# Kernel optimization log

Hardware: AMD Instinct MI355X
Metric: run time of the kernel (lower is better)

## Reference

```python
import jax, jax.numpy as jnp
import numpy as np
from jax import lax

V, VE, DE, DX, HID, T, S = 100000, 1000, 256, 64, 512, 64, 2048
H = HID // 2


def setup_inputs() -> dict:
    key = jax.random.key(0)
    ks = jax.random.split(key, 18)
    def n(k, shape, scale=0.1):
        return jax.random.normal(k, shape, jnp.float32) * scale
    return {
        "sentence": jax.random.randint(ks[0], (S,), 0, V),
        "extra": jax.random.randint(ks[1], (S,), 0, VE),
        "b": 0,
        "e": S,
        "emb": n(ks[2], (V, DE)),
        "extra_emb": n(ks[3], (VE, DX)),
        "w_ih_f": n(ks[4], (4 * H, DE + DX)),
        "w_hh_f": n(ks[5], (4 * H, H)),
        "b_ih_f": n(ks[6], (4 * H,)),
        "b_hh_f": n(ks[7], (4 * H,)),
        "w_ih_b": n(ks[8], (4 * H, DE + DX)),
        "w_hh_b": n(ks[9], (4 * H, H)),
        "b_ih_b": n(ks[10], (4 * H,)),
        "b_hh_b": n(ks[11], (4 * H,)),
        "fc_w": n(ks[12], (T, HID)),
        "fc_b": n(ks[13], (T,)),
        "crf_start": n(ks[14], (T,)),
        "crf_end": n(ks[15], (T,)),
        "crf_trans": n(ks[16], (T, T)),
    }


def _lstm_dir(x, w_ih, w_hh, b_ih, b_hh):
    """Single-direction LSTM over x [S, D] with batch 1. PyTorch gate order i,f,g,o."""
    Hh = w_hh.shape[1]
    gx = x @ w_ih.T + (b_ih + b_hh)  # [S, 4H], input projection hoisted out of the scan

    def step(carry, g_in):
        h, c = carry
        g = g_in + h @ w_hh.T  # [4H]
        i, f, gg, o = jnp.split(g, 4)
        i = jax.nn.sigmoid(i)
        f = jax.nn.sigmoid(f)
        gg = jnp.tanh(gg)
        o = jax.nn.sigmoid(o)
        c = f * c + i * gg
        h = o * jnp.tanh(c)
        return (h, c), h

    init = (jnp.zeros((Hh,), x.dtype), jnp.zeros((Hh,), x.dtype))
    _, hs = lax.scan(step, init, gx)
    return hs  # [S, H]


def _lstm_feats(sentence, extra, emb, extra_emb,
                w_ih_f, w_hh_f, b_ih_f, b_hh_f,
                w_ih_b, w_hh_b, b_ih_b, b_hh_b, fc_w, fc_b):
    x = jnp.concatenate([emb[sentence], extra_emb[extra]], axis=1)  # [S, DE+DX]
    hf = _lstm_dir(x, w_ih_f, w_hh_f, b_ih_f, b_hh_f)              # [S, H]
    hb = _lstm_dir(x[::-1], w_ih_b, w_hh_b, b_ih_b, b_hh_b)[::-1]  # [S, H]
    lstm_out = jnp.concatenate([hf, hb], axis=1)                   # [S, 2H]
    return lstm_out @ fc_w.T + fc_b                                # [S, T]


def _viterbi_decode(feats, start, end, trans):
    """torchcrf-style Viterbi on feats [L, T]; returns best tag path [L] (int32)."""
    score0 = start + feats[0]  # [T]

    def step(score, emit_t):
        m = score[:, None] + trans + emit_t[None, :]  # [T_prev, T_next]
        return jnp.max(m, axis=0), jnp.argmax(m, axis=0).astype(jnp.int32)

    final_score, bps = lax.scan(step, score0, feats[1:])  # bps: [L-1, T]
    final_score = final_score + end
    last_tag = jnp.argmax(final_score).astype(jnp.int32)

    def back(tag, bp_t):
        prev = bp_t[tag]
        return prev, prev

    _, prev_tags = lax.scan(back, last_tag, bps[::-1])
    return jnp.concatenate([prev_tags[::-1], last_tag[None]])  # [L]


def reference(sentence, extra, b, e, emb, extra_emb,
              w_ih_f, w_hh_f, b_ih_f, b_hh_f,
              w_ih_b, w_hh_b, b_ih_b, b_hh_b,
              fc_w, fc_b, crf_start, crf_end, crf_trans):
    feats = _lstm_feats(sentence, extra, emb, extra_emb,
                        w_ih_f, w_hh_f, b_ih_f, b_hh_f,
                        w_ih_b, w_hh_b, b_ih_b, b_hh_b, fc_w, fc_b)
    feats = feats[b:e]  # static Python-int phrase bounds
    return _viterbi_decode(feats, crf_start, crf_end, crf_trans)
```

## Files before the change

kernel.cpp:

```cpp
#include <hip/hip_runtime.h>
#include <stdint.h>

#define SEQ   2048
#define DE    256
#define DXX   64
#define DIN   320
#define HH    256
#define G4    1024
#define NT    64

static constexpr size_t OFF_GX = 0;
static constexpr size_t OFF_H  = OFF_GX + (size_t)2 * SEQ * G4;
static constexpr size_t HSTR   = (size_t)SEQ * HH;
static constexpr size_t OFF_SL = OFF_H + 2 * HSTR;
static constexpr size_t OFF_FE = OFF_SL + 2048;
static constexpr size_t OFF_BP = OFF_FE + (size_t)SEQ * NT;
static constexpr size_t WS_NEEDED_BYTES = OFF_BP * 4 + (size_t)SEQ * NT;

__global__ __launch_bounds__(256) void k_init(unsigned long long* __restrict__ slot) {
  const int tid = threadIdx.x;
  #pragma unroll
  for (int b = 0; b < 4; ++b) slot[b * 256 + tid] = 0ull;
}

__global__ __launch_bounds__(512) void k_gx(
    const int* __restrict__ sent, const int* __restrict__ extra,
    const float* __restrict__ emb, const float* __restrict__ xemb,
    const float* __restrict__ wf, const float* __restrict__ wb,
    const float* __restrict__ bif, const float* __restrict__ bhf,
    const float* __restrict__ bib, const float* __restrict__ bhb,
    float* __restrict__ GX) {
  __shared__ __align__(16) float xs[32][36];
  __shared__ __align__(16) float wl[32][260];
  const int tid = threadIdx.x;
  const int s0 = blockIdx.x * 32, r0 = blockIdx.y * 256, dir = blockIdx.z;
  const float* W = dir ? wb : wf;
  const int tids = tid & 7;
  const int tidr = tid >> 3;
  float acc[4][4];
  #pragma unroll
  for (int a = 0; a < 4; ++a)
    #pragma unroll
    for (int b = 0; b < 4; ++b) acc[a][b] = 0.f;

  for (int kc = 0; kc < 10; ++kc) {
    const int k0 = kc * 32;
    __syncthreads();
    for (int e = tid; e < 1024; e += 512) {
      int kk = e & 31, sl = e >> 5;
      int s = s0 + sl;
      int src = dir ? (SEQ - 1 - s) : s;
      int k = k0 + kk;
      float v;
      if (k < DE) v = emb[(size_t)sent[src] * DE + k];
      else        v = xemb[(size_t)extra[src] * DXX + (k - DE)];
      xs[kk][sl] = v;
    }
    for (int e = tid; e < 8192; e += 512) {
      int kk = e & 31, rl = e >> 5;
      wl[kk][rl] = W[(size_t)(r0 + rl) * DIN + k0 + kk];
    }
    __syncthreads();
    #pragma unroll
    for (int kk = 0; kk < 32; ++kk) {
      float4 xv = *(const float4*)&xs[kk][4 * tids];
      float4 wv = *(const float4*)&wl[kk][4 * tidr];
      acc[0][0] += xv.x * wv.x; acc[0][1] += xv.x * wv.y; acc[0][2] += xv.x * wv.z; acc[0][3] += xv.x * wv.w;
      acc[1][0] += xv.y * wv.x; acc[1][1] += xv.y * wv.y; acc[1][2] += xv.y * wv.z; acc[1][3] += xv.y * wv.w;
      acc[2][0] += xv.z * wv.x; acc[2][1] += xv.z * wv.y; acc[2][2] += xv.z * wv.z; acc[2][3] += xv.z * wv.w;
      acc[3][0] += xv.w * wv.x; acc[3][1] += xv.w * wv.y; acc[3][2] += xv.w * wv.z; acc[3][3] += xv.w * wv.w;
    }
  }
  const float* BI = dir ? bib : bif;
  const float* BH = dir ? bhb : bhf;
  float4 b1 = *(const float4*)&BI[r0 + 4 * tidr];
  float4 b2 = *(const float4*)&BH[r0 + 4 * tidr];
  float bx = b1.x + b2.x, by = b1.y + b2.y, bz = b1.z + b2.z, bw = b1.w + b2.w;
  #pragma unroll
  for (int ss = 0; ss < 4; ++ss) {
    int s = s0 + 4 * tids + ss;
    float4 o;
    o.x = acc[ss][0] + bx; o.y = acc[ss][1] + by; o.z = acc[ss][2] + bz; o.w = acc[ss][3] + bw;
    *(float4*)&GX[((size_t)dir * SEQ + s) * G4 + r0 + 4 * tidr] = o;
  }
}

__global__ __launch_bounds__(256, 1) void k_lstm16(
    const float* __restrict__ whf, const float* __restrict__ whb,
    const float* __restrict__ GX, float* __restrict__ H,
    unsigned long long* __restrict__ slot) {
  const int dir = blockIdx.x >> 4;
  const int p   = blockIdx.x & 15;
  const int tid = threadIdx.x;
  const int rr  = tid >> 2;
  const int q   = tid & 3;
  const int gq  = rr >> 4;
  const int joq = rr & 15;
  const int rowQ = (gq << 8) | (p << 4) | joq;
  const int rowC = ((tid >> 4) << 8) | (p << 4) | (tid & 15);

  const float4* w4g =
      (const float4*)((dir ? whb : whf) + (size_t)rowQ * HH) + q * 16;
  float4 w[16];
  #pragma unroll
  for (int i = 0; i < 16; ++i) w[i] = w4g[i];
  #pragma unroll
  for (int i = 0; i < 16; ++i)
    asm volatile("" : "+v"(w[i].x), "+v"(w[i].y), "+v"(w[i].z), "+v"(w[i].w));

  const float* gxc = GX + (size_t)dir * SEQ * G4 + rowC;
  float* Hd = H + (size_t)dir * HSTR;
  unsigned long long* sl = slot + dir * 512;

  __shared__ __align__(16) float hl[4][68];
  __shared__ float psum[256];
  float c = 0.f;
  int budget = 1 << 18;
  const bool ownpoll = ((tid >> 4) == p);

  if (ownpoll) hl[tid >> 6][tid & 63] = 0.f;

  for (int t = 0; t < SEQ; ++t) {
    float gxv = 0.f;
    if (tid < 64) gxv = gxc[(size_t)t * G4];
    if (!ownpoll) {
      unsigned long long* sp = &sl[(t & 1) * 256 + tid];
      const unsigned tw = (unsigned)t;
      unsigned long long v;
      unsigned long long v0 = __hip_atomic_load(sp, __ATOMIC_RELAXED, __HIP_MEMORY_SCOPE_AGENT);
      unsigned long long v1 = __hip_atomic_load(sp, __ATOMIC_RELAXED, __HIP_MEMORY_SCOPE_AGENT);
      unsigned long long v2 = __hip_atomic_load(sp, __ATOMIC_RELAXED, __HIP_MEMORY_SCOPE_AGENT);
      unsigned long long v3 = __hip_atomic_load(sp, __ATOMIC_RELAXED, __HIP_MEMORY_SCOPE_AGENT);
      for (;;) {
        if ((unsigned)(v0 >> 32) == tw) { v = v0; break; }
        v0 = __hip_atomic_load(sp, __ATOMIC_RELAXED, __HIP_MEMORY_SCOPE_AGENT);
        if ((unsigned)(v1 >> 32) == tw) { v = v1; break; }
        v1 = __hip_atomic_load(sp, __ATOMIC_RELAXED, __HIP_MEMORY_SCOPE_AGENT);
        if ((unsigned)(v2 >> 32) == tw) { v = v2; break; }
        v2 = __hip_atomic_load(sp, __ATOMIC_RELAXED, __HIP_MEMORY_SCOPE_AGENT);
        if ((unsigned)(v3 >> 32) == tw) { v = v3; break; }
        v3 = __hip_atomic_load(sp, __ATOMIC_RELAXED, __HIP_MEMORY_SCOPE_AGENT);
        if (--budget <= 0) { v = v3; break; }
      }
      union { unsigned u; float f; } cv; cv.u = (unsigned)v;
      hl[tid >> 6][tid & 63] = cv.f;
    }
    __syncthreads();
    const float4* h4 = (const float4*)(hl[q]);
    float a0 = 0.f, a1 = 0.f, a2 = 0.f, a3 = 0.f;
    #pragma unroll
    for (int i = 0; i < 16; ++i) {
      float4 wv = w[i];
      float4 hv = h4[i];
      a0 += wv.x * hv.x; a1 += wv.y * hv.y; a2 += wv.z * hv.z; a3 += wv.w * hv.w;
    }
    psum[tid] = (a0 + a1) + (a2 + a3);
    __syncthreads();
    if (tid < 64) {
      float s = gxv + ((psum[4 * tid] + psum[4 * tid + 1]) +
                       (psum[4 * tid + 2] + psum[4 * tid + 3]));
      const int gg_ = tid >> 4;
      const int ee  = tid & 15;
      float sig = 1.f / (1.f + expf(-s));
      float th  = tanhf(s);
      float gated = (gg_ == 2) ? th : sig;
      float fg = __shfl(gated, 16 + ee);
      float gv = __shfl(gated, 32 + ee);
      float og = __shfl(gated, 48 + ee);
      if (tid < 16) {
        c = fg * c + gated * gv;
        float h = og * tanhf(c);
        int jj = (p << 4) | tid;
        union { float f; unsigned u; } hu; hu.f = h;
        unsigned long long pk =
            ((unsigned long long)(unsigned)(t + 1) << 32) | hu.u;
        __hip_atomic_store(&sl[((t + 1) & 1) * 256 + jj], pk, __ATOMIC_RELAXED,
                           __HIP_MEMORY_SCOPE_AGENT);
        hl[jj >> 6][jj & 63] = h;
        Hd[(size_t)t * HH + jj] = h;
      }
    }
  }
}

__global__ __launch_bounds__(256) void k_feats(
    const float* __restrict__ HF, const float* __restrict__ HB,
    const float* __restrict__ fcw, const float* __restrict__ fcb,
    float* __restrict__ FE) {
  __shared__ float hlds[16][512];
  __shared__ float wl[64][65];
  const int tid = threadIdx.x;
  const int s0 = blockIdx.x * 16;
  for (int e = tid; e < 16 * 512; e += 256) {
    int sl = e >> 9, k = e & 511;
    float v = (k < HH) ? HF[(size_t)(s0 + sl) * HH + k]
                       : HB[(size_t)(SEQ - 1 - (s0 + sl)) * HH + (k - HH)];
    hlds[sl][k] = v;
  }
  const int j = tid & 63, sg = tid >> 6;
  float acc[4];
  #pragma unroll
  for (int q = 0; q < 4; ++q) acc[q] = fcb[j];
  for (int kc = 0; kc < 8; ++kc) {
    __syncthreads();
    for (int e = tid; e < 4096; e += 256) {
      int kk = e & 63, jj = e >> 6;
      wl[kk][jj] = fcw[(size_t)jj * 512 + kc * 64 + kk];
    }
    __syncthreads();
    #pragma unroll 8
    for (int kk = 0; kk < 64; ++kk) {
      float wv = wl[kk][j];
      int kg = kc * 64 + kk;
      #pragma unroll
      for (int q = 0; q < 4; ++q) acc[q] += hlds[4 * sg + q][kg] * wv;
    }
  }
  #pragma unroll
  for (int q = 0; q < 4; ++q)
    FE[(size_t)(s0 + 4 * sg + q) * NT + j] = acc[q];
}

__global__ __launch_bounds__(256) void k_viterbi(
    const float* __restrict__ feats, const float* __restrict__ start,
    const float* __restrict__ endv, const float* __restrict__ trans,
    unsigned char* __restrict__ bp, int* __restrict__ out) {
  __shared__ float tr[64 * 64];
  __shared__ float sc[64];
  __shared__ float pval[4][64];
  __shared__ int pidx[4][64];
  const int tid = threadIdx.x;
  for (int e = tid; e < 4096; e += 256) tr[e] = trans[e];
  if (tid < 64) sc[tid] = start[tid] + feats[tid];
  __syncthreads();
  const int w = tid >> 6, j = tid & 63;
  for (int t = 1; t < SEQ; ++t) {
    float fj = feats[t * NT + j];
    float best = -3.0e38f; int bi = 0;
    const int ibase = w << 4;
    #pragma unroll
    for (int ii = 0; ii < 16; ++ii) {
      int i = ibase + ii;
      float v = (sc[i] + tr[(i << 6) | j]) + fj;
      if (v > best) { best = v; bi = i; }
    }
    pval[w][j] = best; pidx[w][j] = bi;
    __syncthreads();
    if (w == 0) {
      float b = pval[0][j]; int x = pidx[0][j];
      if (pval[1][j] > b) { b = pval[1][j]; x = pidx[1][j]; }
      if (pval[2][j] > b) { b = pval[2][j]; x = pidx[2][j]; }
      if (pval[3][j] > b) { b = pval[3][j]; x = pidx[3][j]; }
      bp[t * NT + j] = (unsigned char)x;
      sc[j] = b;
    }
    __syncthreads();
  }
  if (tid == 0) {
    float best = -3.0e38f; int bt = 0;
    for (int i = 0; i < 64; ++i) {
      float v = sc[i] + endv[i];
      if (v > best) { best = v; bt = i; }
    }
    out[SEQ - 1] = bt;
    int tag = bt;
    for (int t = SEQ - 1; t >= 1; --t) {
      tag = bp[t * NT + tag];
      out[t - 1] = tag;
    }
  }
}

extern "C" void kernel_launch(void* const* d_in, const int* in_sizes, int n_in,
                              void* d_out, int out_size, void* d_ws, size_t ws_size,
                              hipStream_t stream) {
  if (n_in < 19) return;
  if (in_sizes[0] != SEQ || in_sizes[1] != SEQ) return;
  if (in_sizes[2] != 1 || in_sizes[3] != 1) return;
  if (in_sizes[4] != 100000 * DE) return;
  if (in_sizes[5] != 1000 * DXX) return;
  if (in_sizes[6] != G4 * DIN || in_sizes[7] != G4 * HH) return;
  if (in_sizes[8] != G4 || in_sizes[9] != G4) return;
  if (in_sizes[10] != G4 * DIN || in_sizes[11] != G4 * HH) return;
  if (in_sizes[14] != NT * 512 || in_sizes[15] != NT) return;
  if (in_sizes[16] != NT || in_sizes[17] != NT) return;
  if (in_sizes[18] != NT * NT) return;
  if (out_size < SEQ) return;
  if (ws_size < WS_NEEDED_BYTES) return;

  const int*   sent = (const int*)d_in[0];
  const int*   extra = (const int*)d_in[1];
  const float* emb  = (const float*)d_in[4];
  const float* xemb = (const float*)d_in[5];
  const float* wihf = (const float*)d_in[6];
  const float* whhf = (const float*)d_in[7];
  const float* bihf = (const float*)d_in[8];
  const float* bhhf = (const float*)d_in[9];
  const float* wihb = (const float*)d_in[10];
  const float* whhb = (const float*)d_in[11];
  const float* bihb = (const float*)d_in[12];
  const float* bhhb = (const float*)d_in[13];
  const float* fcw  = (const float*)d_in[14];
  const float* fcb  = (const float*)d_in[15];
  const float* cst  = (const float*)d_in[16];
  const float* cen  = (const float*)d_in[17];
  const float* ctr  = (const float*)d_in[18];

  float* ws = (float*)d_ws;
  float* GX = ws + OFF_GX;
  float* H  = ws + OFF_H;
  unsigned long long* SLOT = (unsigned long long*)(ws + OFF_SL);
  float* FE = ws + OFF_FE;
  unsigned char* BP = (unsigned char*)(ws + OFF_BP);

  k_init<<<1, 256, 0, stream>>>(SLOT);
  k_gx<<<dim3(SEQ / 32, G4 / 256, 2), 512, 0, stream>>>(
      sent, extra, emb, xemb, wihf, wihb, bihf, bhhf, bihb, bhhb, GX);
  k_lstm16<<<32, 256, 0, stream>>>(whhf, whhb, GX, H, SLOT);
  k_feats<<<SEQ / 16, 256, 0, stream>>>(H, H + HSTR, fcw, fcb, FE);
  k_viterbi<<<1, 256, 0, stream>>>(FE, cst, cen, ctr, BP, (int*)d_out);
}
```

Measured before the change: 4.984 ms.

## Move LSTM gate math to wave 3, split polling, cheapen barriers, stage Viterbi backtrace in LDS

The LSTM step now polls remote hidden-state slots with two slots per thread in waves 0-2 plus part of wave 3, and runs the gate nonlinearity on wave 3. This spreads polling latency across the waves. Barriers are replaced with a waitcnt-lgkm-only s_barrier, which skips waiting on outstanding global memory operations. The Viterbi kernel prefetches the next step's emission and copies backpointer chunks into LDS before the serial backtrace, so each hop avoids a dependent global load. The weaker barrier relies on global atomics and stores not needing completion at the barrier, and the backtrace adds extra block syncs per chunk.

```diff
diff --git a/kernel.cpp b/kernel.cpp
--- a/kernel.cpp
+++ b/kernel.cpp
@@ -16,6 +16,10 @@
 static constexpr size_t OFF_FE = OFF_SL + 2048;
 static constexpr size_t OFF_BP = OFF_FE + (size_t)SEQ * NT;
 static constexpr size_t WS_NEEDED_BYTES = OFF_BP * 4 + (size_t)SEQ * NT;
+
+__device__ __forceinline__ void bar_lds() {
+  asm volatile("s_waitcnt lgkmcnt(0)\n\ts_barrier" ::: "memory");
+}
 
 __global__ __launch_bounds__(256) void k_init(unsigned long long* __restrict__ slot) {
   const int tid = threadIdx.x;
@@ -97,7 +101,6 @@
   const int gq  = rr >> 4;
   const int joq = rr & 15;
   const int rowQ = (gq << 8) | (p << 4) | joq;
-  const int rowC = ((tid >> 4) << 8) | (p << 4) | (tid & 15);
 
   const float4* w4g =
       (const float4*)((dir ? whb : whf) + (size_t)rowQ * HH) + q * 16;
@@ -108,6 +111,9 @@
   for (int i = 0; i < 16; ++i)
     asm volatile("" : "+v"(w[i].x), "+v"(w[i].y), "+v"(w[i].z), "+v"(w[i].w));
 
+  const bool isw3 = (tid >= 192);
+  const int cc = tid & 63;
+  const int rowC = ((cc >> 4) << 8) | (p << 4) | (cc & 15);
   const float* gxc = GX + (size_t)dir * SEQ * G4 + rowC;
   float* Hd = H + (size_t)dir * HSTR;
   unsigned long long* sl = slot + dir * 512;
@@ -116,36 +122,43 @@
   __shared__ float psum[256];
   float c = 0.f;
   int budget = 1 << 18;
-  const bool ownpoll = ((tid >> 4) == p);
-
-  if (ownpoll) hl[tid >> 6][tid & 63] = 0.f;
+
+  const int s1 = tid;
+  const int s2 = 192 + tid;
+  const bool need1 = !isw3 && ((s1 >> 4) != p);
+  const bool need2 = (tid < 64) && ((s2 >> 4) != p);
+
+  if (isw3 && cc < 16) {
+    int jj = (p << 4) | cc;
+    hl[jj >> 6][jj & 63] = 0.f;
+  }
 
   for (int t = 0; t < SEQ; ++t) {
     float gxv = 0.f;
-    if (tid < 64) gxv = gxc[(size_t)t * G4];
-    if (!ownpoll) {
-      unsigned long long* sp = &sl[(t & 1) * 256 + tid];
+    if (isw3) gxv = gxc[(size_t)t * G4];
+    if (need1 | need2) {
       const unsigned tw = (unsigned)t;
-      unsigned long long v;
-      unsigned long long v0 = __hip_atomic_load(sp, __ATOMIC_RELAXED, __HIP_MEMORY_SCOPE_AGENT);
-      unsigned long long v1 = __hip_atomic_load(sp, __ATOMIC_RELAXED, __HIP_MEMORY_SCOPE_AGENT);
-      unsigned long long v2 = __hip_atomic_load(sp, __ATOMIC_RELAXED, __HIP_MEMORY_SCOPE_AGENT);
-      unsigned long long v3 = __hip_atomic_load(sp, __ATOMIC_RELAXED, __HIP_MEMORY_SCOPE_AGENT);
-      for (;;) {
-        if ((unsigned)(v0 >> 32) == tw) { v = v0; break; }
-        v0 = __hip_atomic_load(sp, __ATOMIC_RELAXED, __HIP_MEMORY_SCOPE_AGENT);
-        if ((unsigned)(v1 >> 32) == tw) { v = v1; break; }
-        v1 = __hip_atomic_load(sp, __ATOMIC_RELAXED, __HIP_MEMORY_SCOPE_AGENT);
-        if ((unsigned)(v2 >> 32) == tw) { v = v2; break; }
-        v2 = __hip_atomic_load(sp, __ATOMIC_RELAXED, __HIP_MEMORY_SCOPE_AGENT);
-        if ((unsigned)(v3 >> 32) == tw) { v = v3; break; }
-        v3 = __hip_atomic_load(sp, __ATOMIC_RELAXED, __HIP_MEMORY_SCOPE_AGENT);
-        if (--budget <= 0) { v = v3; break; }
-      }
-      union { unsigned u; float f; } cv; cv.u = (unsigned)v;
-      hl[tid >> 6][tid & 63] = cv.f;
-    }
-    __syncthreads();
+      unsigned long long* sp1 = &sl[(t & 1) * 256 + s1];
+      unsigned long long* sp2 = &sl[(t & 1) * 256 + s2];
+      bool d1 = !need1, d2 = !need2;
+      do {
+        if (!d1) {
+          unsigned long long v = __hip_atomic_load(sp1, __ATOMIC_RELAXED, __HIP_MEMORY_SCOPE_AGENT);
+          if ((unsigned)(v >> 32) == tw) {
+            union { unsigned u; float f; } cv; cv.u = (unsigned)v;
+            hl[s1 >> 6][s1 & 63] = cv.f; d1 = true;
+          }
+        }
+        if (!d2) {
+          unsigned long long v = __hip_atomic_load(sp2, __ATOMIC_RELAXED, __HIP_MEMORY_SCOPE_AGENT);
+          if ((unsigned)(v >> 32) == tw) {
+            union { unsigned u; float f; } cv; cv.u = (unsigned)v;
+            hl[s2 >> 6][s2 & 63] = cv.f; d2 = true;
+          }
+        }
+      } while (!(d1 && d2) && --budget > 0);
+    }
+    bar_lds();
     const float4* h4 = (const float4*)(hl[q]);
     float a0 = 0.f, a1 = 0.f, a2 = 0.f, a3 = 0.f;
     #pragma unroll
@@ -155,22 +168,22 @@
       a0 += wv.x * hv.x; a1 += wv.y * hv.y; a2 += wv.z * hv.z; a3 += wv.w * hv.w;
     }
     psum[tid] = (a0 + a1) + (a2 + a3);
-    __syncthreads();
-    if (tid < 64) {
-      float s = gxv + ((psum[4 * tid] + psum[4 * tid + 1]) +
-                       (psum[4 * tid + 2] + psum[4 * tid + 3]));
-      const int gg_ = tid >> 4;
-      const int ee  = tid & 15;
+    bar_lds();
+    if (isw3) {
+      float s = gxv + ((psum[4 * cc] + psum[4 * cc + 1]) +
+                       (psum[4 * cc + 2] + psum[4 * cc + 3]));
+      const int gg_ = cc >> 4;
+      const int ee  = cc & 15;
       float sig = 1.f / (1.f + expf(-s));
       float th  = tanhf(s);
       float gated = (gg_ == 2) ? th : sig;
       float fg = __shfl(gated, 16 + ee);
       float gv = __shfl(gated, 32 + ee);
       float og = __shfl(gated, 48 + ee);
-      if (tid < 16) {
+      if (cc < 16) {
         c = fg * c + gated * gv;
         float h = og * tanhf(c);
-        int jj = (p << 4) | tid;
+        int jj = (p << 4) | cc;
         union { float f; unsigned u; } hu; hu.f = h;
         unsigned long long pk =
             ((unsigned long long)(unsigned)(t + 1) << 32) | hu.u;
@@ -229,13 +242,16 @@
   __shared__ float sc[64];
   __shared__ float pval[4][64];
   __shared__ int pidx[4][64];
+  __shared__ unsigned char bpl[64][64];
   const int tid = threadIdx.x;
   for (int e = tid; e < 4096; e += 256) tr[e] = trans[e];
   if (tid < 64) sc[tid] = start[tid] + feats[tid];
   __syncthreads();
   const int w = tid >> 6, j = tid & 63;
+  float fj_cur = feats[1 * NT + j];
   for (int t = 1; t < SEQ; ++t) {
-    float fj = feats[t * NT + j];
+    float fj = fj_cur;
+    if (t + 1 < SEQ) fj_cur = feats[(t + 1) * NT + j];
     float best = -3.0e38f; int bi = 0;
     const int ibase = w << 4;
     #pragma unroll
@@ -245,7 +261,7 @@
       if (v > best) { best = v; bi = i; }
     }
     pval[w][j] = best; pidx[w][j] = bi;
-    __syncthreads();
+    bar_lds();
     if (w == 0) {
       float b = pval[0][j]; int x = pidx[0][j];
       if (pval[1][j] > b) { b = pval[1][j]; x = pidx[1][j]; }
@@ -254,8 +270,10 @@
       bp[t * NT + j] = (unsigned char)x;
       sc[j] = b;
     }
-    __syncthreads();
-  }
+    bar_lds();
+  }
+  __syncthreads();
+  __shared__ int btag;
   if (tid == 0) {
     float best = -3.0e38f; int bt = 0;
     for (int i = 0; i < 64; ++i) {
@@ -263,10 +281,26 @@
       if (v > best) { best = v; bt = i; }
     }
     out[SEQ - 1] = bt;
-    int tag = bt;
-    for (int t = SEQ - 1; t >= 1; --t) {
-      tag = bp[t * NT + tag];
-      out[t - 1] = tag;
+    btag = bt;
+  }
+  __syncthreads();
+  int tag = btag;
+  for (int cchunk = 31; cchunk >= 0; --cchunk) {
+    const int tbase = cchunk * 64;
+    __syncthreads();
+    for (int wd = tid; wd < 1024; wd += 256)
+      ((unsigned int*)bpl)[wd] =
+          ((const unsigned int*)bp)[tbase * 16 + wd];
+    __syncthreads();
+    if (tid == 0) {
+      #pragma unroll 4
+      for (int k = 63; k >= 0; --k) {
+        int t = tbase + k;
+        if (t >= 1) {
+          tag = bpl[k][tag];
+          out[t - 1] = tag;
+        }
+      }
     }
   }
 }
```

Result: slower. 5.446 ms (+9.3%).

## Stage Viterbi backpointers in LDS chunks and add sleep-based LSTM polling

Applied to the files above, without the earlier changes.

The Viterbi kernel now keeps backpointers in a 64-step LDS buffer and writes them to global memory in cooperative chunks. The backtrace reloads each chunk into LDS before a single thread walks it, which avoids a serial chain of dependent global loads. It also prefetches the next emission row and replaces __syncthreads with a bare lgkmcnt wait plus s_barrier. Separately, the LSTM spin-wait now uses two alternating loads with s_sleep in place of four back-to-back loads, which lowers memory pressure from polling but may add wake-up latency on every timestep.

```diff
diff --git a/kernel.cpp b/kernel.cpp
--- a/kernel.cpp
+++ b/kernel.cpp
@@ -16,6 +16,10 @@
 static constexpr size_t OFF_FE = OFF_SL + 2048;
 static constexpr size_t OFF_BP = OFF_FE + (size_t)SEQ * NT;
 static constexpr size_t WS_NEEDED_BYTES = OFF_BP * 4 + (size_t)SEQ * NT;
+
+__device__ __forceinline__ void bar_lds() {
+  asm volatile("s_waitcnt lgkmcnt(0)\n\ts_barrier" ::: "memory");
+}
 
 __global__ __launch_bounds__(256) void k_init(unsigned long long* __restrict__ slot) {
   const int tid = threadIdx.x;
@@ -127,20 +131,15 @@
       unsigned long long* sp = &sl[(t & 1) * 256 + tid];
       const unsigned tw = (unsigned)t;
       unsigned long long v;
-      unsigned long long v0 = __hip_atomic_load(sp, __ATOMIC_RELAXED, __HIP_MEMORY_SCOPE_AGENT);
-      unsigned long long v1 = __hip_atomic_load(sp, __ATOMIC_RELAXED, __HIP_MEMORY_SCOPE_AGENT);
-      unsigned long long v2 = __hip_atomic_load(sp, __ATOMIC_RELAXED, __HIP_MEMORY_SCOPE_AGENT);
-      unsigned long long v3 = __hip_atomic_load(sp, __ATOMIC_RELAXED, __HIP_MEMORY_SCOPE_AGENT);
+      unsigned long long vA = __hip_atomic_load(sp, __ATOMIC_RELAXED, __HIP_MEMORY_SCOPE_AGENT);
       for (;;) {
-        if ((unsigned)(v0 >> 32) == tw) { v = v0; break; }
-        v0 = __hip_atomic_load(sp, __ATOMIC_RELAXED, __HIP_MEMORY_SCOPE_AGENT);
-        if ((unsigned)(v1 >> 32) == tw) { v = v1; break; }
-        v1 = __hip_atomic_load(sp, __ATOMIC_RELAXED, __HIP_MEMORY_SCOPE_AGENT);
-        if ((unsigned)(v2 >> 32) == tw) { v = v2; break; }
-        v2 = __hip_atomic_load(sp, __ATOMIC_RELAXED, __HIP_MEMORY_SCOPE_AGENT);
-        if ((unsigned)(v3 >> 32) == tw) { v = v3; break; }
-        v3 = __hip_atomic_load(sp, __ATOMIC_RELAXED, __HIP_MEMORY_SCOPE_AGENT);
-        if (--budget <= 0) { v = v3; break; }
+        __builtin_amdgcn_s_sleep(2);
+        unsigned long long vB = __hip_atomic_load(sp, __ATOMIC_RELAXED, __HIP_MEMORY_SCOPE_AGENT);
+        if ((unsigned)(vA >> 32) == tw) { v = vA; break; }
+        if (--budget <= 0) { v = vA; break; }
+        __builtin_amdgcn_s_sleep(2);
+        vA = __hip_atomic_load(sp, __ATOMIC_RELAXED, __HIP_MEMORY_SCOPE_AGENT);
+        if ((unsigned)(vB >> 32) == tw) { v = vB; break; }
       }
       union { unsigned u; float f; } cv; cv.u = (unsigned)v;
       hl[tid >> 6][tid & 63] = cv.f;
@@ -229,13 +228,17 @@
   __shared__ float sc[64];
   __shared__ float pval[4][64];
   __shared__ int pidx[4][64];
+  __shared__ __align__(16) unsigned char bpb[64][64];
+  __shared__ int btag;
   const int tid = threadIdx.x;
   for (int e = tid; e < 4096; e += 256) tr[e] = trans[e];
   if (tid < 64) sc[tid] = start[tid] + feats[tid];
   __syncthreads();
   const int w = tid >> 6, j = tid & 63;
+  float fj_cur = feats[NT + j];
   for (int t = 1; t < SEQ; ++t) {
-    float fj = feats[t * NT + j];
+    float fj = fj_cur;
+    if (t + 1 < SEQ) fj_cur = feats[(t + 1) * NT + j];
     float best = -3.0e38f; int bi = 0;
     const int ibase = w << 4;
     #pragma unroll
@@ -245,17 +248,24 @@
       if (v > best) { best = v; bi = i; }
     }
     pval[w][j] = best; pidx[w][j] = bi;
-    __syncthreads();
+    bar_lds();
     if (w == 0) {
       float b = pval[0][j]; int x = pidx[0][j];
       if (pval[1][j] > b) { b = pval[1][j]; x = pidx[1][j]; }
       if (pval[2][j] > b) { b = pval[2][j]; x = pidx[2][j]; }
       if (pval[3][j] > b) { b = pval[3][j]; x = pidx[3][j]; }
-      bp[t * NT + j] = (unsigned char)x;
+      bpb[t & 63][j] = (unsigned char)x;
       sc[j] = b;
     }
-    __syncthreads();
-  }
+    bar_lds();
+    if ((t & 63) == 63) {
+      const int tbase = t & ~63;
+      for (int wd = tid; wd < 1024; wd += 256)
+        ((unsigned int*)bp)[tbase * 16 + wd] = ((const unsigned int*)bpb)[wd];
+      bar_lds();
+    }
+  }
+  __syncthreads();
   if (tid == 0) {
     float best = -3.0e38f; int bt = 0;
     for (int i = 0; i < 64; ++i) {
@@ -263,10 +273,25 @@
       if (v > best) { best = v; bt = i; }
     }
     out[SEQ - 1] = bt;
-    int tag = bt;
-    for (int t = SEQ - 1; t >= 1; --t) {
-      tag = bp[t * NT + tag];
-      out[t - 1] = tag;
+    btag = bt;
+  }
+  __syncthreads();
+  int tag = btag;
+  for (int cchunk = 31; cchunk >= 0; --cchunk) {
+    const int tbase = cchunk * 64;
+    __syncthreads();
+    for (int wd = tid; wd < 1024; wd += 256)
+      ((unsigned int*)bpb)[wd] = ((const unsigned int*)bp)[tbase * 16 + wd];
+    __syncthreads();
+    if (tid == 0) {
+      #pragma unroll 4
+      for (int k = 63; k >= 0; --k) {
+        int t = tbase + k;
+        if (t >= 1) {
+          tag = bpb[k][tag];
+          out[t - 1] = tag;
+        }
+      }
     }
   }
 }
```

Result: slower. 5.481 ms (+10.0%).
